# Kernel optimization log

Measured on AMD Instinct MI355X. Metric: run time of the kernel, lower is better.

Reference implementation:

```python
import jax, jax.numpy as jnp
import numpy as np

B, T, C = 2, 2048, 768
H = 12
D = C // H  # head size = 64
F = 4 * C
EPS = 1e-5


def _layernorm(x, g, b):
    mu = jnp.mean(x, axis=-1, keepdims=True)
    var = jnp.var(x, axis=-1, keepdims=True)
    return (x - mu) * jax.lax.rsqrt(var + EPS) * g + b


def setup_inputs() -> dict:
    key = jax.random.key(0)
    ks = jax.random.split(key, 16)
    s_in = 1.0 / np.sqrt(C)
    s_ff = 1.0 / np.sqrt(F)
    return {
        "x": jax.random.normal(ks[0], (B, T, C), dtype=jnp.float32),
        # per-head projection weights, stacked [H, C, D] (no bias, as in nn.Linear(bias=False))
        "Wq": jax.random.uniform(ks[1], (H, C, D), jnp.float32, -s_in, s_in),
        "Wk": jax.random.uniform(ks[2], (H, C, D), jnp.float32, -s_in, s_in),
        "Wv": jax.random.uniform(ks[3], (H, C, D), jnp.float32, -s_in, s_in),
        "Wp": jax.random.uniform(ks[4], (C, C), jnp.float32, -s_in, s_in),
        "bp": jax.random.uniform(ks[5], (C,), jnp.float32, -s_in, s_in),
        "W1": jax.random.uniform(ks[6], (C, F), jnp.float32, -s_in, s_in),
        "b1": jax.random.uniform(ks[7], (F,), jnp.float32, -s_in, s_in),
        "W2": jax.random.uniform(ks[8], (F, C), jnp.float32, -s_ff, s_ff),
        "b2": jax.random.uniform(ks[9], (C,), jnp.float32, -s_ff, s_ff),
        "ln1_g": jnp.ones((C,), jnp.float32),
        "ln1_b": jnp.zeros((C,), jnp.float32),
        "ln2_g": jnp.ones((C,), jnp.float32),
        "ln2_b": jnp.zeros((C,), jnp.float32),
    }


def reference(x, Wq, Wk, Wv, Wp, bp, W1, b1, W2, b2, ln1_g, ln1_b, ln2_g, ln2_b):
    # --- self-attention sublayer (pre-LN) ---
    h = _layernorm(x, ln1_g, ln1_b)                      # [B,T,C]
    q = jnp.einsum('btc,hcd->bhtd', h, Wq)
    k = jnp.einsum('btc,hcd->bhtd', h, Wk)
    v = jnp.einsum('btc,hcd->bhtd', h, Wv)
    # NOTE: original scales by C**-0.5 where C = n_embd (full width), not head size
    scale = C ** (-0.5)
    wei = jnp.einsum('bhtd,bhsd->bhts', q, k) * scale    # [B,H,T,T]
    causal = jnp.tril(jnp.ones((T, T), dtype=bool))
    wei = jnp.where(causal, wei, -jnp.inf)
    wei = jax.nn.softmax(wei, axis=-1)
    out = jnp.einsum('bhts,bhsd->bhtd', wei, v)          # [B,H,T,D]
    out = out.transpose(0, 2, 1, 3).reshape(B, T, C)     # concat heads
    sa = out @ Wp + bp
    x = x + sa
    # --- feed-forward sublayer (pre-LN); ReLU after BOTH linears, as in source ---
    h2 = _layernorm(x, ln2_g, ln2_b)
    ff = jax.nn.relu(jax.nn.relu(h2 @ W1 + b1) @ W2 + b2)
    return x + ff
```

## Files before the change

### kernel.cpp

```cpp
#include <hip/hip_runtime.h>
#include <hip/hip_bf16.h>

#define TSEQ 2048
#define CDIM 768
#define NHEAD 12
#define DHEAD 64
#define FDIM 3072
#define MROWS 4096
#define BH 24

typedef __attribute__((ext_vector_type(8))) short short8;
typedef __attribute__((ext_vector_type(4))) float f32x4;

__device__ inline unsigned short f2bf(float f) {
  __hip_bfloat16 h = __float2bfloat16(f);
  return __builtin_bit_cast(unsigned short, h);
}
__device__ inline float bf2f(unsigned short u) {
  unsigned int v = ((unsigned int)u) << 16;
  return __builtin_bit_cast(float, v);
}

__device__ inline void gload16(const unsigned short* g, unsigned short* l) {
  __builtin_amdgcn_global_load_lds(
      (const __attribute__((address_space(1))) unsigned int*)g,
      (__attribute__((address_space(3))) unsigned int*)l, 16, 0, 0);
}

__global__ __launch_bounds__(256) void prep_all(
    const float* __restrict__ Wq, const float* __restrict__ Wk,
    const float* __restrict__ Wv, const float* __restrict__ Wp,
    const float* __restrict__ W1, const float* __restrict__ W2,
    unsigned short* __restrict__ WqkvT, unsigned short* __restrict__ WpT,
    unsigned short* __restrict__ W1T, unsigned short* __restrict__ W2T,
    const float* __restrict__ x, const float* __restrict__ ln1g,
    const float* __restrict__ ln1b, unsigned short* __restrict__ h1) {
  __shared__ float tile[32][33];
  __shared__ float red[8];
  int b = blockIdx.x;
  if (b >= 6912) {
    int row = b - 6912;
    int tid = threadIdx.x;
    const float* xr = x + (size_t)row * CDIM;
    float v[3];
    float s = 0.f;
#pragma unroll
    for (int i = 0; i < 3; ++i) { v[i] = xr[tid + i * 256]; s += v[i]; }
#pragma unroll
    for (int m = 1; m < 64; m <<= 1) s += __shfl_xor(s, m);
    int w = tid >> 6;
    if ((tid & 63) == 0) red[w] = s;
    __syncthreads();
    float mean = (red[0] + red[1] + red[2] + red[3]) * (1.f / CDIM);
    float vs = 0.f;
#pragma unroll
    for (int i = 0; i < 3; ++i) { float d = v[i] - mean; vs += d * d; }
#pragma unroll
    for (int m = 1; m < 64; m <<= 1) vs += __shfl_xor(vs, m);
    if ((tid & 63) == 0) red[4 + w] = vs;
    __syncthreads();
    float var = (red[4] + red[5] + red[6] + red[7]) * (1.f / CDIM);
    float rstd = rsqrtf(var + 1e-5f);
    unsigned short* orow = h1 + (size_t)row * CDIM;
#pragma unroll
    for (int i = 0; i < 3; ++i) {
      int c = tid + i * 256;
      orow[c] = f2bf((v[i] - mean) * rstd * ln1g[c] + ln1b[c]);
    }
    return;
  }
  int xx = threadIdx.x & 31, y = threadIdx.x >> 5;
  if (b < 1728) {
    int cx = b % 24, dy = (b / 24) % 2, ph = b / 48;
    int proj = ph / NHEAD, h = ph % NHEAD;
    const float* in = (proj == 0 ? Wq : (proj == 1 ? Wk : Wv)) + (size_t)h * CDIM * DHEAD;
    int c0 = cx * 32, d0 = dy * 32;
#pragma unroll
    for (int i = 0; i < 4; ++i)
      tile[y + i * 8][xx] = in[(size_t)(c0 + y + i * 8) * DHEAD + d0 + xx];
    __syncthreads();
#pragma unroll
    for (int i = 0; i < 4; ++i)
      WqkvT[(size_t)(proj * CDIM + h * DHEAD + d0 + y + i * 8) * CDIM + c0 + xx] =
          f2bf(tile[xx][y + i * 8]);
  } else {
    const float* in;
    unsigned short* out;
    int R, C, bx, by;
    if (b < 2304) {
      int b2 = b - 1728;
      in = Wp; out = WpT; R = CDIM; C = CDIM; bx = b2 % 24; by = b2 / 24;
    } else if (b < 4608) {
      int b2 = b - 2304;
      in = W1; out = W1T; R = CDIM; C = FDIM; bx = b2 % 96; by = b2 / 96;
    } else {
      int b2 = b - 4608;
      in = W2; out = W2T; R = FDIM; C = CDIM; bx = b2 % 24; by = b2 / 24;
    }
    int c0 = bx * 32, r0 = by * 32;
#pragma unroll
    for (int i = 0; i < 4; ++i)
      tile[y + i * 8][xx] = in[(size_t)(r0 + y + i * 8) * C + c0 + xx];
    __syncthreads();
#pragma unroll
    for (int i = 0; i < 4; ++i)
      out[(size_t)(c0 + y + i * 8) * R + r0 + xx] = f2bf(tile[xx][y + i * 8]);
  }
}

__global__ __launch_bounds__(256) void redln(
    const unsigned short* __restrict__ part,
    const float* __restrict__ bias, const float* __restrict__ x,
    float* __restrict__ x1, const float* __restrict__ g,
    const float* __restrict__ bb, unsigned short* __restrict__ h2) {
  int row = blockIdx.x;
  int tid = threadIdx.x;
  float v[3];
  float s = 0.f;
#pragma unroll
  for (int i = 0; i < 3; ++i) {
    int c = tid + i * 256;
    size_t idx = (size_t)row * CDIM + c;
    float t = bf2f(part[idx]) + bf2f(part[(size_t)MROWS * CDIM + idx]) + bias[c] + x[idx];
    v[i] = t;
    x1[idx] = t;
    s += t;
  }
#pragma unroll
  for (int m = 1; m < 64; m <<= 1) s += __shfl_xor(s, m);
  __shared__ float red[8];
  int w = tid >> 6;
  if ((tid & 63) == 0) red[w] = s;
  __syncthreads();
  float mean = (red[0] + red[1] + red[2] + red[3]) * (1.f / CDIM);
  float vs = 0.f;
#pragma unroll
  for (int i = 0; i < 3; ++i) { float d = v[i] - mean; vs += d * d; }
#pragma unroll
  for (int m = 1; m < 64; m <<= 1) vs += __shfl_xor(vs, m);
  if ((tid & 63) == 0) red[4 + w] = vs;
  __syncthreads();
  float var = (red[4] + red[5] + red[6] + red[7]) * (1.f / CDIM);
  float rstd = rsqrtf(var + 1e-5f);
  unsigned short* orow = h2 + (size_t)row * CDIM;
#pragma unroll
  for (int i = 0; i < 3; ++i) {
    int c = tid + i * 256;
    orow[c] = f2bf((v[i] - mean) * rstd * g[c] + bb[c]);
  }
}

template <int EPI, int SPLITK = 1>
__global__ __launch_bounds__(256) void gemm_bt(
    const unsigned short* __restrict__ A, const unsigned short* __restrict__ BT,
    int M, int N, int K,
    const float* __restrict__ bias, const float* __restrict__ aux,
    float* __restrict__ outf, unsigned short* __restrict__ outb,
    unsigned short* __restrict__ qo, unsigned short* __restrict__ ko,
    unsigned short* __restrict__ vo) {
  constexpr int SH_CNT = (EPI == 0) ? 128 * 136 : 2 * 128 * 64;
  __shared__ unsigned short sh[SH_CNT];
  unsigned short* As = sh;
  unsigned short* Bs = sh + 128 * 64;
  int tid = threadIdx.x;
  int lane = tid & 63, wave = tid >> 6;
  int wr = wave >> 1, wc = wave & 1;
  int l15 = lane & 15, lg = lane >> 4;
  int lr = lane >> 3, lc = lane & 7;
  int chunk = gridDim.x >> 3;
  int logical = (blockIdx.x & 7) * chunk + (blockIdx.x >> 3);
  int mt = M >> 7;
  int tiles = mt * (N >> 7);
  int split = logical / tiles;
  int tl = logical % tiles;
  size_t bm = (size_t)(tl % mt) * 128, bn = (size_t)(tl / mt) * 128;
  int Ks = K / SPLITK;
  int kbeg = split * Ks, kend = kbeg + Ks;
  f32x4 acc[4][4] = {};

  for (int kt = kbeg; kt < kend; kt += 64) {
#pragma unroll
    for (int i = 0; i < 4; ++i) {
      int r0 = (wave * 4 + i) * 8;
      gload16(A + (bm + r0 + lr) * K + kt + (lc ^ lr) * 8, &As[r0 * 64]);
      gload16(BT + (bn + r0 + lr) * K + kt + (lc ^ lr) * 8, &Bs[r0 * 64]);
    }
    __syncthreads();
    __builtin_amdgcn_s_setprio(1);
#pragma unroll
    for (int kk = 0; kk < 64; kk += 32) {
      int kb = kk + lg * 8;
      short8 af[4], bfr[4];
#pragma unroll
      for (int m = 0; m < 4; ++m) {
        int row = wr * 64 + m * 16 + l15;
        af[m] = *reinterpret_cast<const short8*>(&As[row * 64 + (kb ^ ((row & 7) << 3))]);
      }
#pragma unroll
      for (int n = 0; n < 4; ++n) {
        int row = wc * 64 + n * 16 + l15;
        bfr[n] = *reinterpret_cast<const short8*>(&Bs[row * 64 + (kb ^ ((row & 7) << 3))]);
      }
#pragma unroll
      for (int m = 0; m < 4; ++m)
#pragma unroll
        for (int n = 0; n < 4; ++n)
          acc[m][n] = __builtin_amdgcn_mfma_f32_16x16x32_bf16(af[m], bfr[n], acc[m][n], 0, 0, 0);
    }
    __builtin_amdgcn_s_setprio(0);
    __syncthreads();
  }

  if constexpr (EPI == 0) {
    if (bn >= 1536) {
#pragma unroll
      for (int m = 0; m < 4; ++m)
#pragma unroll
        for (int n = 0; n < 4; ++n)
#pragma unroll
          for (int r = 0; r < 4; ++r) {
            int rowL = wr * 64 + m * 16 + lg * 4 + r;
            int c = wc * 64 + n * 16 + l15;
            sh[c * 136 + rowL] = f2bf(acc[m][n][r]);
          }
      __syncthreads();
      int bb = (int)(bm >> 11);
      int t0g = (int)(bm & 2047);
      int vbase = (int)bn - 1536;
#pragma unroll
      for (int it = 0; it < 8; ++it) {
        int ch = it * 256 + tid;
        int c = ch >> 4, tlc = (ch & 15) * 8;
        int vcol = vbase + c;
        int hh = vcol >> 6, dd = vcol & 63;
        *reinterpret_cast<int4*>(
            vo + (((size_t)(bb * NHEAD + hh)) * DHEAD + dd) * TSEQ + t0g + tlc) =
            *reinterpret_cast<const int4*>(&sh[c * 136 + tlc]);
      }
    } else {
#pragma unroll
      for (int m = 0; m < 4; ++m)
#pragma unroll
        for (int n = 0; n < 4; ++n)
#pragma unroll
          for (int r = 0; r < 4; ++r) {
            int row = (int)bm + wr * 64 + m * 16 + lg * 4 + r;
            int col = (int)bn + wc * 64 + n * 16 + l15;
            float val = acc[m][n][r];
            int proj = col / CDIM, rem = col % CDIM;
            int h = rem >> 6, d = rem & 63;
            int b = row >> 11, t = row & (TSEQ - 1);
            if (proj == 0) {
              qo[(((size_t)(b * NHEAD + h)) * TSEQ + t) * DHEAD + d] =
                  f2bf(val * 0.05205877247186126f);
            } else {
              ko[(((size_t)(b * NHEAD + h)) * TSEQ + t) * DHEAD + d] = f2bf(val);
            }
          }
    }
  } else {
#pragma unroll
    for (int m = 0; m < 4; ++m) {
#pragma unroll
      for (int n = 0; n < 4; ++n) {
#pragma unroll
        for (int r = 0; r < 4; ++r) {
          int row = (int)bm + wr * 64 + m * 16 + lg * 4 + r;
          int col = (int)bn + wc * 64 + n * 16 + l15;
          float val = acc[m][n][r];
          if constexpr (EPI == 1) {
            size_t idx = (size_t)row * CDIM + col;
            outf[idx] = val + bias[col] + aux[idx];
          } else if constexpr (EPI == 2) {
            size_t idx = (size_t)row * FDIM + col;
            outb[idx] = f2bf(fmaxf(val + bias[col], 0.f));
          } else if constexpr (EPI == 3) {
            size_t idx = (size_t)row * CDIM + col;
            outf[idx] = aux[idx] + fmaxf(val + bias[col], 0.f);
          } else {
            outb[(size_t)split * M * N + (size_t)row * N + col] = f2bf(val);
          }
        }
      }
    }
  }
}

template <int NPART, bool RELU>
__global__ __launch_bounds__(256) void reduce_k(
    const unsigned short* __restrict__ part,
    const float* __restrict__ bias, const float* __restrict__ aux,
    float* __restrict__ out) {
  int e = (blockIdx.x * 256 + threadIdx.x) * 4;
  int col = e % CDIM;
  float4 xv = *reinterpret_cast<const float4*>(aux + e);
  float4 bv = *reinterpret_cast<const float4*>(bias + col);
  float s0 = 0.f, s1 = 0.f, s2 = 0.f, s3 = 0.f;
#pragma unroll
  for (int p = 0; p < NPART; ++p) {
    short4 pv = *reinterpret_cast<const short4*>(part + (size_t)p * MROWS * CDIM + e);
    s0 += bf2f((unsigned short)pv.x);
    s1 += bf2f((unsigned short)pv.y);
    s2 += bf2f((unsigned short)pv.z);
    s3 += bf2f((unsigned short)pv.w);
  }
  float4 ov;
  if constexpr (RELU) {
    ov.x = xv.x + fmaxf(s0 + bv.x, 0.f);
    ov.y = xv.y + fmaxf(s1 + bv.y, 0.f);
    ov.z = xv.z + fmaxf(s2 + bv.z, 0.f);
    ov.w = xv.w + fmaxf(s3 + bv.w, 0.f);
  } else {
    ov.x = xv.x + s0 + bv.x;
    ov.y = xv.y + s1 + bv.y;
    ov.z = xv.z + s2 + bv.z;
    ov.w = xv.w + s3 + bv.w;
  }
  *reinterpret_cast<float4*>(out + e) = ov;
}

__global__ __launch_bounds__(128) void attn_kernel(
    const unsigned short* __restrict__ Q, const unsigned short* __restrict__ Kd,
    const unsigned short* __restrict__ VT, unsigned short* __restrict__ O) {
  __shared__ unsigned short Kl[2][64 * 64];
  __shared__ unsigned short Vl[2][64 * 64];
  __shared__ unsigned short plds[2][16 * 64];
  int tid = threadIdx.x;
  int wave = tid >> 6, lane = tid & 63;
  int l15 = lane & 15, lg = lane >> 4;
  int bid = blockIdx.x;
  int xcd = bid & 7, idx = bid >> 3;
  int bh = xcd * 3 + idx % 3;
  int stripe = 63 - idx / 3;
  const unsigned short* qp = Q + (size_t)bh * TSEQ * DHEAD;
  const unsigned short* kp = Kd + (size_t)bh * TSEQ * DHEAD;
  const unsigned short* vp = VT + (size_t)bh * DHEAD * TSEQ;
  unsigned short* pw = plds[wave];
  int b = bh / NHEAD, h = bh % NHEAD;

  short8 ones;
  {
    unsigned short ov = (l15 == 0) ? (unsigned short)0x3F80 : (unsigned short)0;
#pragma unroll
    for (int j = 0; j < 8; ++j) ones[j] = (short)ov;
  }

  int lr = lane >> 3, lc = lane & 7;
  int jsw = lc ^ lr;

  auto stage = [&](int t, int buf) {
    int s0 = t * 64;
#pragma unroll
    for (int i = 0; i < 4; ++i) {
      int r0 = (wave * 4 + i) * 8;
      gload16(kp + (size_t)(s0 + r0 + lr) * DHEAD + jsw * 8, &Kl[buf][r0 * 64]);
      gload16(vp + (size_t)(r0 + lr) * TSEQ + s0 + jsw * 8, &Vl[buf][r0 * 64]);
    }
  };

  int qbase = stripe * 32 + wave * 16;
  int nt = (stripe >> 1) + 1;
  short8 qf[2];
#pragma unroll
  for (int kk = 0; kk < 2; ++kk)
    qf[kk] = *reinterpret_cast<const short8*>(
        qp + (size_t)(qbase + l15) * DHEAD + kk * 32 + lg * 8);
  f32x4 oacc[5] = {};

  stage(0, 0);
  asm volatile("s_waitcnt vmcnt(0)" ::: "memory");
  __builtin_amdgcn_s_barrier();

  for (int t = 0; t < nt; ++t) {
    int cur = t & 1;
    if (t + 1 < nt) stage(t + 1, cur ^ 1);
    int s0 = t * 64;
    f32x4 sacc[4] = {};
    __builtin_amdgcn_s_setprio(1);
#pragma unroll
    for (int st = 0; st < 4; ++st) {
      int row = st * 16 + l15;
      int sw = row & 7;
#pragma unroll
      for (int kk = 0; kk < 2; ++kk) {
        short8 kf = *reinterpret_cast<const short8*>(
            &Kl[cur][row * 64 + (((kk * 4 + lg) ^ sw) * 8)]);
        sacc[st] = __builtin_amdgcn_mfma_f32_16x16x32_bf16(qf[kk], kf, sacc[st], 0, 0, 0);
      }
    }
    __builtin_amdgcn_s_setprio(0);
    bool last = (t == nt - 1);
#pragma unroll
    for (int r = 0; r < 4; ++r) {
      int qrow = qbase + lg * 4 + r;
      int prow = lg * 4 + r;
      int psw = (prow & 7) << 3;
      if (last) {
#pragma unroll
        for (int st = 0; st < 4; ++st) {
          float pv = exp2f(sacc[st][r]);
          if (s0 + st * 16 + l15 > qrow) pv = 0.f;
          pw[prow * 64 + ((st * 16 + l15) ^ psw)] = f2bf(pv);
        }
      } else {
#pragma unroll
        for (int st = 0; st < 4; ++st)
          pw[prow * 64 + ((st * 16 + l15) ^ psw)] = f2bf(exp2f(sacc[st][r]));
      }
    }
    int prsw = (l15 & 7) << 3;
    short8 pa0 = *reinterpret_cast<const short8*>(&pw[l15 * 64 + ((lg * 8) ^ prsw)]);
    short8 pa1 = *reinterpret_cast<const short8*>(&pw[l15 * 64 + ((32 + lg * 8) ^ prsw)]);
    __builtin_amdgcn_s_setprio(1);
#pragma unroll
    for (int n = 0; n < 4; ++n) {
      int row = n * 16 + l15;
      int sw = row & 7;
      short8 vf0 = *reinterpret_cast<const short8*>(&Vl[cur][row * 64 + ((lg ^ sw) * 8)]);
      oacc[n] = __builtin_amdgcn_mfma_f32_16x16x32_bf16(pa0, vf0, oacc[n], 0, 0, 0);
      short8 vf1 = *reinterpret_cast<const short8*>(&Vl[cur][row * 64 + (((4 + lg) ^ sw) * 8)]);
      oacc[n] = __builtin_amdgcn_mfma_f32_16x16x32_bf16(pa1, vf1, oacc[n], 0, 0, 0);
    }
    oacc[4] = __builtin_amdgcn_mfma_f32_16x16x32_bf16(pa0, ones, oacc[4], 0, 0, 0);
    oacc[4] = __builtin_amdgcn_mfma_f32_16x16x32_bf16(pa1, ones, oacc[4], 0, 0, 0);
    __builtin_amdgcn_s_setprio(0);
    asm volatile("s_waitcnt vmcnt(0)" ::: "memory");
    __builtin_amdgcn_s_barrier();
  }

#pragma unroll
  for (int r = 0; r < 4; ++r) {
    float lsum = __shfl(oacc[4][r], lane & 48);
    float inv = 1.f / lsum;
    int row = qbase + lg * 4 + r;
#pragma unroll
    for (int n = 0; n < 4; ++n)
      O[(size_t)(b * TSEQ + row) * CDIM + h * DHEAD + n * 16 + l15] =
          f2bf(oacc[n][r] * inv);
  }
}

extern "C" void kernel_launch(void* const* d_in, const int* in_sizes, int n_in,
                              void* d_out, int out_size, void* d_ws, size_t ws_size,
                              hipStream_t stream) {
  const float* x    = (const float*)d_in[0];
  const float* Wq   = (const float*)d_in[1];
  const float* Wk   = (const float*)d_in[2];
  const float* Wv   = (const float*)d_in[3];
  const float* Wp   = (const float*)d_in[4];
  const float* bp   = (const float*)d_in[5];
  const float* W1   = (const float*)d_in[6];
  const float* b1   = (const float*)d_in[7];
  const float* W2   = (const float*)d_in[8];
  const float* b2   = (const float*)d_in[9];
  const float* ln1g = (const float*)d_in[10];
  const float* ln1b = (const float*)d_in[11];
  const float* ln2g = (const float*)d_in[12];
  const float* ln2b = (const float*)d_in[13];
  float* out = (float*)d_out;

  char* ws = (char*)d_ws;
  auto alloc = [&](size_t bytes) {
    char* p = ws;
    ws += (bytes + 255) & ~(size_t)255;
    return p;
  };
  unsigned short* h1    = (unsigned short*)alloc((size_t)MROWS * CDIM * 2);
  unsigned short* WqkvT = (unsigned short*)alloc((size_t)3 * CDIM * CDIM * 2);
  unsigned short* WpT   = (unsigned short*)alloc((size_t)CDIM * CDIM * 2);
  unsigned short* W1T   = (unsigned short*)alloc((size_t)FDIM * CDIM * 2);
  unsigned short* W2T   = (unsigned short*)alloc((size_t)CDIM * FDIM * 2);
  unsigned short* Qb    = (unsigned short*)alloc((size_t)BH * TSEQ * DHEAD * 2);
  unsigned short* Kb    = (unsigned short*)alloc((size_t)BH * TSEQ * DHEAD * 2);
  unsigned short* VTb   = (unsigned short*)alloc((size_t)BH * TSEQ * DHEAD * 2);
  unsigned short* AO    = (unsigned short*)alloc((size_t)MROWS * CDIM * 2);
  float*          x1    = (float*)alloc((size_t)MROWS * CDIM * 4);
  unsigned short* h2    = (unsigned short*)alloc((size_t)MROWS * CDIM * 2);
  unsigned short* a1    = (unsigned short*)alloc((size_t)MROWS * FDIM * 2);
  unsigned short* partP = Qb;

  prep_all<<<11008, 256, 0, stream>>>(Wq, Wk, Wv, Wp, W1, W2,
                                      WqkvT, WpT, W1T, W2T, x, ln1g, ln1b, h1);
  gemm_bt<0><<<576, 256, 0, stream>>>(h1, WqkvT, MROWS, 3 * CDIM, CDIM,
                                      nullptr, nullptr, nullptr, nullptr, Qb, Kb, VTb);
  attn_kernel<<<1536, 128, 0, stream>>>(Qb, Kb, VTb, AO);
  gemm_bt<4, 2><<<384, 256, 0, stream>>>(AO, WpT, MROWS, CDIM, CDIM,
                                         nullptr, nullptr, nullptr, partP,
                                         nullptr, nullptr, nullptr);
  redln<<<4096, 256, 0, stream>>>(partP, bp, x, x1, ln2g, ln2b, h2);
  gemm_bt<2><<<768, 256, 0, stream>>>(h2, W1T, MROWS, FDIM, CDIM,
                                      b1, nullptr, nullptr, a1, nullptr, nullptr, nullptr);
  gemm_bt<4, 4><<<768, 256, 0, stream>>>(a1, W2T, MROWS, CDIM, FDIM,
                                         nullptr, nullptr, nullptr, partP,
                                         nullptr, nullptr, nullptr);
  reduce_k<4, true><<<3072, 256, 0, stream>>>(partP, b2, x1, out);
}
```

Baseline: 159.7 us.

## Double attention query rows per wave to reuse K/V tiles across two row groups

Each attention block now handles a 64-row query stripe, with each wave covering 32 rows (two 16-row groups) instead of 16. Every K and V fragment read from LDS is fed to two MFMAs, which halves K/V staging traffic and LDS reads per query row. The grid halves to 768 blocks. In exchange, registers per thread rise (doubled accumulators and Q fragments), the causal-diagonal tile wastes more work, and fewer blocks leave coarser load balance across CUs.

Result: slower. 186.1 us (+16.6%).

```diff
diff --git a/kernel.cpp b/kernel.cpp
--- a/kernel.cpp
+++ b/kernel.cpp
@@ -324,14 +324,14 @@
     const unsigned short* __restrict__ VT, unsigned short* __restrict__ O) {
   __shared__ unsigned short Kl[2][64 * 64];
   __shared__ unsigned short Vl[2][64 * 64];
-  __shared__ unsigned short plds[2][16 * 64];
+  __shared__ unsigned short plds[2][32 * 64];
   int tid = threadIdx.x;
   int wave = tid >> 6, lane = tid & 63;
   int l15 = lane & 15, lg = lane >> 4;
   int bid = blockIdx.x;
   int xcd = bid & 7, idx = bid >> 3;
   int bh = xcd * 3 + idx % 3;
-  int stripe = 63 - idx / 3;
+  int stripe = 31 - idx / 3;
   const unsigned short* qp = Q + (size_t)bh * TSEQ * DHEAD;
   const unsigned short* kp = Kd + (size_t)bh * TSEQ * DHEAD;
   const unsigned short* vp = VT + (size_t)bh * DHEAD * TSEQ;
@@ -358,14 +358,16 @@
     }
   };
 
-  int qbase = stripe * 32 + wave * 16;
-  int nt = (stripe >> 1) + 1;
-  short8 qf[2];
-#pragma unroll
-  for (int kk = 0; kk < 2; ++kk)
-    qf[kk] = *reinterpret_cast<const short8*>(
-        qp + (size_t)(qbase + l15) * DHEAD + kk * 32 + lg * 8);
-  f32x4 oacc[5] = {};
+  int qbase = stripe * 64 + wave * 32;
+  int nt = stripe + 1;
+  short8 qf[2][2];
+#pragma unroll
+  for (int rg = 0; rg < 2; ++rg)
+#pragma unroll
+    for (int kk = 0; kk < 2; ++kk)
+      qf[rg][kk] = *reinterpret_cast<const short8*>(
+          qp + (size_t)(qbase + rg * 16 + l15) * DHEAD + kk * 32 + lg * 8);
+  f32x4 oacc[2][5] = {};
 
   stage(0, 0);
   asm volatile("s_waitcnt vmcnt(0)" ::: "memory");
@@ -375,7 +377,7 @@
     int cur = t & 1;
     if (t + 1 < nt) stage(t + 1, cur ^ 1);
     int s0 = t * 64;
-    f32x4 sacc[4] = {};
+    f32x4 sacc[2][4] = {};
     __builtin_amdgcn_s_setprio(1);
 #pragma unroll
     for (int st = 0; st < 4; ++st) {
@@ -385,58 +387,75 @@
       for (int kk = 0; kk < 2; ++kk) {
         short8 kf = *reinterpret_cast<const short8*>(
             &Kl[cur][row * 64 + (((kk * 4 + lg) ^ sw) * 8)]);
-        sacc[st] = __builtin_amdgcn_mfma_f32_16x16x32_bf16(qf[kk], kf, sacc[st], 0, 0, 0);
+        sacc[0][st] = __builtin_amdgcn_mfma_f32_16x16x32_bf16(qf[0][kk], kf, sacc[0][st], 0, 0, 0);
+        sacc[1][st] = __builtin_amdgcn_mfma_f32_16x16x32_bf16(qf[1][kk], kf, sacc[1][st], 0, 0, 0);
       }
     }
     __builtin_amdgcn_s_setprio(0);
     bool last = (t == nt - 1);
 #pragma unroll
-    for (int r = 0; r < 4; ++r) {
-      int qrow = qbase + lg * 4 + r;
-      int prow = lg * 4 + r;
-      int psw = (prow & 7) << 3;
-      if (last) {
-#pragma unroll
-        for (int st = 0; st < 4; ++st) {
-          float pv = exp2f(sacc[st][r]);
-          if (s0 + st * 16 + l15 > qrow) pv = 0.f;
-          pw[prow * 64 + ((st * 16 + l15) ^ psw)] = f2bf(pv);
+    for (int rg = 0; rg < 2; ++rg) {
+#pragma unroll
+      for (int r = 0; r < 4; ++r) {
+        int qrow = qbase + rg * 16 + lg * 4 + r;
+        int prow = rg * 16 + lg * 4 + r;
+        int psw = (prow & 7) << 3;
+        if (last) {
+#pragma unroll
+          for (int st = 0; st < 4; ++st) {
+            float pv = exp2f(sacc[rg][st][r]);
+            if (s0 + st * 16 + l15 > qrow) pv = 0.f;
+            pw[prow * 64 + ((st * 16 + l15) ^ psw)] = f2bf(pv);
+          }
+        } else {
+#pragma unroll
+          for (int st = 0; st < 4; ++st)
+            pw[prow * 64 + ((st * 16 + l15) ^ psw)] = f2bf(exp2f(sacc[rg][st][r]));
         }
-      } else {
-#pragma unroll
-        for (int st = 0; st < 4; ++st)
-          pw[prow * 64 + ((st * 16 + l15) ^ psw)] = f2bf(exp2f(sacc[st][r]));
       }
     }
     int prsw = (l15 & 7) << 3;
-    short8 pa0 = *reinterpret_cast<const short8*>(&pw[l15 * 64 + ((lg * 8) ^ prsw)]);
-    short8 pa1 = *reinterpret_cast<const short8*>(&pw[l15 * 64 + ((32 + lg * 8) ^ prsw)]);
+    short8 pa0[2], pa1[2];
+#pragma unroll
+    for (int rg = 0; rg < 2; ++rg) {
+      pa0[rg] = *reinterpret_cast<const short8*>(
+          &pw[(rg * 16 + l15) * 64 + ((lg * 8) ^ prsw)]);
+      pa1[rg] = *reinterpret_cast<const short8*>(
+          &pw[(rg * 16 + l15) * 64 + ((32 + lg * 8) ^ prsw)]);
+    }
     __builtin_amdgcn_s_setprio(1);
 #pragma unroll
     for (int n = 0; n < 4; ++n) {
       int row = n * 16 + l15;
       int sw = row & 7;
       short8 vf0 = *reinterpret_cast<const short8*>(&Vl[cur][row * 64 + ((lg ^ sw) * 8)]);
-      oacc[n] = __builtin_amdgcn_mfma_f32_16x16x32_bf16(pa0, vf0, oacc[n], 0, 0, 0);
       short8 vf1 = *reinterpret_cast<const short8*>(&Vl[cur][row * 64 + (((4 + lg) ^ sw) * 8)]);
-      oacc[n] = __builtin_amdgcn_mfma_f32_16x16x32_bf16(pa1, vf1, oacc[n], 0, 0, 0);
-    }
-    oacc[4] = __builtin_amdgcn_mfma_f32_16x16x32_bf16(pa0, ones, oacc[4], 0, 0, 0);
-    oacc[4] = __builtin_amdgcn_mfma_f32_16x16x32_bf16(pa1, ones, oacc[4], 0, 0, 0);
+      oacc[0][n] = __builtin_amdgcn_mfma_f32_16x16x32_bf16(pa0[0], vf0, oacc[0][n], 0, 0, 0);
+      oacc[0][n] = __builtin_amdgcn_mfma_f32_16x16x32_bf16(pa1[0], vf1, oacc[0][n], 0, 0, 0);
+      oacc[1][n] = __builtin_amdgcn_mfma_f32_16x16x32_bf16(pa0[1], vf0, oacc[1][n], 0, 0, 0);
+      oacc[1][n] = __builtin_amdgcn_mfma_f32_16x16x32_bf16(pa1[1], vf1, oacc[1][n], 0, 0, 0);
+    }
+    oacc[0][4] = __builtin_amdgcn_mfma_f32_16x16x32_bf16(pa0[0], ones, oacc[0][4], 0, 0, 0);
+    oacc[0][4] = __builtin_amdgcn_mfma_f32_16x16x32_bf16(pa1[0], ones, oacc[0][4], 0, 0, 0);
+    oacc[1][4] = __builtin_amdgcn_mfma_f32_16x16x32_bf16(pa0[1], ones, oacc[1][4], 0, 0, 0);
+    oacc[1][4] = __builtin_amdgcn_mfma_f32_16x16x32_bf16(pa1[1], ones, oacc[1][4], 0, 0, 0);
     __builtin_amdgcn_s_setprio(0);
     asm volatile("s_waitcnt vmcnt(0)" ::: "memory");
     __builtin_amdgcn_s_barrier();
   }
 
 #pragma unroll
-  for (int r = 0; r < 4; ++r) {
-    float lsum = __shfl(oacc[4][r], lane & 48);
-    float inv = 1.f / lsum;
-    int row = qbase + lg * 4 + r;
-#pragma unroll
-    for (int n = 0; n < 4; ++n)
-      O[(size_t)(b * TSEQ + row) * CDIM + h * DHEAD + n * 16 + l15] =
-          f2bf(oacc[n][r] * inv);
+  for (int rg = 0; rg < 2; ++rg) {
+#pragma unroll
+    for (int r = 0; r < 4; ++r) {
+      float lsum = __shfl(oacc[rg][4][r], lane & 48);
+      float inv = 1.f / lsum;
+      int row = qbase + rg * 16 + lg * 4 + r;
+#pragma unroll
+      for (int n = 0; n < 4; ++n)
+        O[(size_t)(b * TSEQ + row) * CDIM + h * DHEAD + n * 16 + l15] =
+            f2bf(oacc[rg][n][r] * inv);
+    }
   }
 }
 
@@ -483,7 +502,7 @@
                                       WqkvT, WpT, W1T, W2T, x, ln1g, ln1b, h1);
   gemm_bt<0><<<576, 256, 0, stream>>>(h1, WqkvT, MROWS, 3 * CDIM, CDIM,
                                       nullptr, nullptr, nullptr, nullptr, Qb, Kb, VTb);
-  attn_kernel<<<1536, 128, 0, stream>>>(Qb, Kb, VTb, AO);
+  attn_kernel<<<768, 128, 0, stream>>>(Qb, Kb, VTb, AO);
   gemm_bt<4, 2><<<384, 256, 0, stream>>>(AO, WpT, MROWS, CDIM, CDIM,
                                          nullptr, nullptr, nullptr, partP,
                                          nullptr, nullptr, nullptr);
```
